# Performance work log

Hardware: AMD Instinct MI355X
Metric: run time of the kernel (lower is better)

The kernel has to match this reference:

```python
import jax, jax.numpy as jnp
import numpy as np

LEN_C = 1024
LR = 0.01
GAMMA = 0.999
R, S, E = 4, 4, 4


def setup_inputs() -> dict:
    key = jax.random.key(0)
    k1, k2, k3 = jax.random.split(key, 3)
    Fx = jax.random.normal(k1, (R, S, E, LEN_C), dtype=jnp.float32)
    Dis = jax.random.normal(k2, (E, LEN_C), dtype=jnp.float32)
    initial_weights = jax.random.normal(k3, (R, S, LEN_C), dtype=jnp.float32) * 0.02
    return {"Fx": Fx, "Dis": Dis, "initial_weights": initial_weights}


def reference(Fx, Dis, initial_weights):
    len_c = Fx.shape[-1]
    # --- first_grad: one-step adaptation gradient (detached in original torch code) ---
    w0 = jax.lax.stop_gradient(initial_weights)
    anti = jnp.einsum('rsen,rsn->e', Fx, w0)           # [E]
    error = Dis[:, -1] - anti                           # [E]
    # d/dw of sum_e error_e^2 with error = Dis - Fx.w  =>  -2 * Fx^T error
    weights_grad = jax.lax.stop_gradient(-2.0 * jnp.einsum('rsen,e->rsn', Fx, error))
    control_weights = initial_weights - 0.5 * LR * weights_grad  # [R,S,N]
    # --- build_delay_line, vectorized Toeplitz gather:
    # Fx_extend[t, r, s, e, n] = Fx[r, s, e, t-n] if t >= n else 0
    t = jnp.arange(len_c)
    idx = t[:, None] - t[None, :]                       # [T, N]
    mask = idx >= 0
    safe_idx = jnp.where(mask, idx, 0)
    Fx_ext = jnp.where(mask, Fx[..., safe_idx], jnp.float32(0.0))  # [R,S,E,T,N]
    # --- adaptive_filtering: sum over r, s, n ---
    anti_noise_matrix = jnp.einsum('rsetn,rsn->te', Fx_ext, control_weights)  # [T,E]
    gamma_vector = jnp.power(jnp.float32(GAMMA), (len_c - 1 - t).astype(jnp.float32))
    return anti_noise_matrix, gamma_vector
```

## Files before the change

kernel.cpp:

```cpp
#include <hip/hip_runtime.h>

#define LEN_C 1024
#define LR_F 0.01f
#define GAMMA_F 0.999f

__global__ __launch_bounds__(256) void k_fused(const float* __restrict__ Fx,
                                               const float* __restrict__ Dis,
                                               const float* __restrict__ w0,
                                               float* __restrict__ out) {
    int bid = blockIdx.x;
    int tid = threadIdx.x;
    int e = bid / 40;
    int r = bid % 40;
    int Tb, Nb;
    if (r < 4)       { Tb = 0; Nb = r; }
    else if (r < 12) { Tb = 1; Nb = r - 4; }
    else if (r < 24) { Tb = 2; Nb = r - 12; }
    else             { Tb = 3; Nb = r - 24; }
    const int T0 = Tb * 256, N0 = Nb * 64;
    const int B = T0 - N0 - 63;

    __shared__ __align__(16) float sFx[16 * 320];
    __shared__ __align__(16) float sCw[16 * 64];
    __shared__ float sPart[4][4];
    __shared__ float sErr[4];

    if (bid < 4) {
        int g = (bid << 8) + tid;
        out[4 * LEN_C + g] = powf(GAMMA_F, (float)(LEN_C - 1 - g));
    }

    for (int rs = 0; rs < 16; ++rs) {
        const float* src = Fx + (rs * 4 + e) * LEN_C;
        for (int m = tid; m < 320; m += 256) {
            int k = B + m;
            sFx[rs * 320 + m] = ((unsigned)k < (unsigned)LEN_C) ? src[k] : 0.f;
        }
    }

    float a0 = 0.f, a1 = 0.f, a2 = 0.f, a3 = 0.f;
    #pragma unroll 4
    for (int i = tid; i < 4096; i += 256) {
        int rs = i >> 8;
        int n4 = i & 255;
        const float4* fx = (const float4*)(Fx + rs * (4 * LEN_C)) + n4;
        float4 wv = ((const float4*)(w0 + rs * LEN_C))[n4];
        float4 f0 = fx[0], f1 = fx[256], f2 = fx[512], f3 = fx[768];
        a0 += f0.x * wv.x + f0.y * wv.y + f0.z * wv.z + f0.w * wv.w;
        a1 += f1.x * wv.x + f1.y * wv.y + f1.z * wv.z + f1.w * wv.w;
        a2 += f2.x * wv.x + f2.y * wv.y + f2.z * wv.z + f2.w * wv.w;
        a3 += f3.x * wv.x + f3.y * wv.y + f3.z * wv.z + f3.w * wv.w;
    }
    for (int off = 32; off > 0; off >>= 1) {
        a0 += __shfl_down(a0, off, 64);
        a1 += __shfl_down(a1, off, 64);
        a2 += __shfl_down(a2, off, 64);
        a3 += __shfl_down(a3, off, 64);
    }
    int w = tid >> 6, l = tid & 63;
    if (l == 0) { sPart[w][0] = a0; sPart[w][1] = a1; sPart[w][2] = a2; sPart[w][3] = a3; }
    __syncthreads();
    if (tid < 4) {
        float anti = sPart[0][tid] + sPart[1][tid] + sPart[2][tid] + sPart[3][tid];
        sErr[tid] = Dis[tid * LEN_C + (LEN_C - 1)] - anti;
    }
    __syncthreads();

    {
        int rs = tid >> 4, j4 = (tid & 15) * 4;
        int n = N0 + j4;
        const float* base = Fx + rs * (4 * LEN_C) + n;
        float4 wv = *(const float4*)(w0 + rs * LEN_C + n);
        float4 f0 = *(const float4*)(base);
        float4 f1 = *(const float4*)(base + LEN_C);
        float4 f2 = *(const float4*)(base + 2 * LEN_C);
        float4 f3 = *(const float4*)(base + 3 * LEN_C);
        float e0 = sErr[0], e1 = sErr[1], e2 = sErr[2], e3 = sErr[3];
        float4 c;
        c.x = wv.x + LR_F * (f0.x * e0 + f1.x * e1 + f2.x * e2 + f3.x * e3);
        c.y = wv.y + LR_F * (f0.y * e0 + f1.y * e1 + f2.y * e2 + f3.y * e3);
        c.z = wv.z + LR_F * (f0.z * e0 + f1.z * e1 + f2.z * e2 + f3.z * e3);
        c.w = wv.w + LR_F * (f0.w * e0 + f1.w * e1 + f2.w * e2 + f3.w * e3);
        *(float4*)(sCw + rs * 64 + j4) = c;
    }
    __syncthreads();

    int i0 = l * 4;
    float acc0 = 0.f, acc1 = 0.f, acc2 = 0.f, acc3 = 0.f;
    #pragma unroll
    for (int rr = 0; rr < 4; ++rr) {
        int rs = (w << 2) + rr;
        const float* crow = sCw + rs * 64;
        const float* frow = sFx + rs * 320;
        int M = i0 + 60;
        float4 flo = *(const float4*)(frow + M);
        float4 fhi = *(const float4*)(frow + M + 4);
        #pragma unroll
        for (int jb = 0; jb < 16; ++jb) {
            float4 c = *(const float4*)(crow + (jb << 2));
            float v0 = flo.x, v1 = flo.y, v2 = flo.z, v3 = flo.w;
            float v4 = fhi.x, v5 = fhi.y, v6 = fhi.z;
            acc0 += v3 * c.x + v2 * c.y + v1 * c.z + v0 * c.w;
            acc1 += v4 * c.x + v3 * c.y + v2 * c.z + v1 * c.w;
            acc2 += v5 * c.x + v4 * c.y + v3 * c.z + v2 * c.w;
            acc3 += v6 * c.x + v5 * c.y + v4 * c.z + v3 * c.w;
            fhi = flo;
            M -= 4;
            if (jb < 15) flo = *(const float4*)(frow + M);
        }
    }

    __syncthreads();
    float* sred = sFx;
    sred[w * 256 + i0 + 0] = acc0;
    sred[w * 256 + i0 + 1] = acc1;
    sred[w * 256 + i0 + 2] = acc2;
    sred[w * 256 + i0 + 3] = acc3;
    __syncthreads();
    float sum = sred[tid] + sred[256 + tid] + sred[512 + tid] + sred[768 + tid];
    atomicAdd(&out[(T0 + tid) * 4 + e], sum);
}

extern "C" void kernel_launch(void* const* d_in, const int* in_sizes, int n_in,
                              void* d_out, int out_size, void* d_ws, size_t ws_size,
                              hipStream_t stream) {
    const float* Fx  = (const float*)d_in[0];
    const float* Dis = (const float*)d_in[1];
    const float* w0  = (const float*)d_in[2];
    float* out = (float*)d_out;

    k_fused<<<160, 256, 0, stream>>>(Fx, Dis, w0, out);
}
```

Baseline: 72.26 us.

## Split fused kernel into single-block prep and 640-block convolution kernel

Moves the error and control-weight computation into a separate one-block kernel that writes the control weights to workspace. The convolution kernel no longer recomputes the global dot-product reduction in every block. It also splits the rs dimension into four groups, so it launches 640 smaller blocks with less shared memory each. The cost is a second kernel launch, a serial dependency on a single-block kernel, and four times as many atomicAdds into the output.

```diff
diff --git a/kernel.cpp b/kernel.cpp
--- a/kernel.cpp
+++ b/kernel.cpp
@@ -4,14 +4,79 @@
 #define LR_F 0.01f
 #define GAMMA_F 0.999f
 
-__global__ __launch_bounds__(256) void k_fused(const float* __restrict__ Fx,
+__global__ __launch_bounds__(1024) void k_prep(const float* __restrict__ Fx,
                                                const float* __restrict__ Dis,
                                                const float* __restrict__ w0,
+                                               float* __restrict__ cw,
                                                float* __restrict__ out) {
-    int bid = blockIdx.x;
-    int tid = threadIdx.x;
-    int e = bid / 40;
-    int r = bid % 40;
+    const int tid = threadIdx.x;
+    const int w = tid >> 6;
+    const int l = tid & 63;
+
+    __shared__ float sP[16][4];
+    __shared__ float sErr[4];
+
+    out[4 * LEN_C + tid] = powf(GAMMA_F, (float)(LEN_C - 1 - tid));
+
+    const float4* wp = (const float4*)(w0 + w * LEN_C);
+    const float4* fp = (const float4*)(Fx + w * 4 * LEN_C);
+    float4 wv[4], fv[4][4];
+    #pragma unroll
+    for (int k = 0; k < 4; ++k) wv[k] = wp[l + 64 * k];
+    #pragma unroll
+    for (int e = 0; e < 4; ++e)
+        #pragma unroll
+        for (int k = 0; k < 4; ++k) fv[e][k] = fp[e * 256 + l + 64 * k];
+
+    float a[4];
+    #pragma unroll
+    for (int e = 0; e < 4; ++e) {
+        float s = 0.f;
+        #pragma unroll
+        for (int k = 0; k < 4; ++k)
+            s += fv[e][k].x * wv[k].x + fv[e][k].y * wv[k].y +
+                 fv[e][k].z * wv[k].z + fv[e][k].w * wv[k].w;
+        a[e] = s;
+    }
+    #pragma unroll
+    for (int off = 32; off > 0; off >>= 1) {
+        a[0] += __shfl_down(a[0], off, 64);
+        a[1] += __shfl_down(a[1], off, 64);
+        a[2] += __shfl_down(a[2], off, 64);
+        a[3] += __shfl_down(a[3], off, 64);
+    }
+    if (l == 0) { sP[w][0] = a[0]; sP[w][1] = a[1]; sP[w][2] = a[2]; sP[w][3] = a[3]; }
+    __syncthreads();
+    if (tid < 4) {
+        float anti = 0.f;
+        #pragma unroll
+        for (int rs = 0; rs < 16; ++rs) anti += sP[rs][tid];
+        sErr[tid] = Dis[tid * LEN_C + (LEN_C - 1)] - anti;
+    }
+    __syncthreads();
+
+    const float e0 = sErr[0], e1 = sErr[1], e2 = sErr[2], e3 = sErr[3];
+    float4* cwp = (float4*)(cw + w * LEN_C);
+    #pragma unroll
+    for (int k = 0; k < 4; ++k) {
+        float4 c;
+        c.x = wv[k].x + LR_F * (fv[0][k].x * e0 + fv[1][k].x * e1 + fv[2][k].x * e2 + fv[3][k].x * e3);
+        c.y = wv[k].y + LR_F * (fv[0][k].y * e0 + fv[1][k].y * e1 + fv[2][k].y * e2 + fv[3][k].y * e3);
+        c.z = wv[k].z + LR_F * (fv[0][k].z * e0 + fv[1][k].z * e1 + fv[2][k].z * e2 + fv[3][k].z * e3);
+        c.w = wv[k].w + LR_F * (fv[0][k].w * e0 + fv[1][k].w * e1 + fv[2][k].w * e2 + fv[3][k].w * e3);
+        cwp[l + 64 * k] = c;
+    }
+}
+
+__global__ __launch_bounds__(256) void k_conv(const float* __restrict__ Fx,
+                                              const float* __restrict__ cw,
+                                              float* __restrict__ out) {
+    const int bid = blockIdx.x;
+    const int tid = threadIdx.x;
+    const int g = bid & 3;
+    const int r = (bid >> 2) % 40;
+    const int e = bid / 160;
+
     int Tb, Nb;
     if (r < 4)       { Tb = 0; Nb = r; }
     else if (r < 12) { Tb = 1; Nb = r - 4; }
@@ -20,78 +85,26 @@
     const int T0 = Tb * 256, N0 = Nb * 64;
     const int B = T0 - N0 - 63;
 
-    __shared__ __align__(16) float sFx[16 * 320];
-    __shared__ __align__(16) float sCw[16 * 64];
-    __shared__ float sPart[4][4];
-    __shared__ float sErr[4];
+    __shared__ __align__(16) float sFx[4 * 320];
+    __shared__ __align__(16) float sCw[4 * 64];
 
-    if (bid < 4) {
-        int g = (bid << 8) + tid;
-        out[4 * LEN_C + g] = powf(GAMMA_F, (float)(LEN_C - 1 - g));
-    }
-
-    for (int rs = 0; rs < 16; ++rs) {
-        const float* src = Fx + (rs * 4 + e) * LEN_C;
+    #pragma unroll
+    for (int rr = 0; rr < 4; ++rr) {
+        const float* src = Fx + ((g * 4 + rr) * 4 + e) * LEN_C;
         for (int m = tid; m < 320; m += 256) {
             int k = B + m;
-            sFx[rs * 320 + m] = ((unsigned)k < (unsigned)LEN_C) ? src[k] : 0.f;
+            sFx[rr * 320 + m] = ((unsigned)k < (unsigned)LEN_C) ? src[k] : 0.f;
         }
     }
-
-    float a0 = 0.f, a1 = 0.f, a2 = 0.f, a3 = 0.f;
-    #pragma unroll 4
-    for (int i = tid; i < 4096; i += 256) {
-        int rs = i >> 8;
-        int n4 = i & 255;
-        const float4* fx = (const float4*)(Fx + rs * (4 * LEN_C)) + n4;
-        float4 wv = ((const float4*)(w0 + rs * LEN_C))[n4];
-        float4 f0 = fx[0], f1 = fx[256], f2 = fx[512], f3 = fx[768];
-        a0 += f0.x * wv.x + f0.y * wv.y + f0.z * wv.z + f0.w * wv.w;
-        a1 += f1.x * wv.x + f1.y * wv.y + f1.z * wv.z + f1.w * wv.w;
-        a2 += f2.x * wv.x + f2.y * wv.y + f2.z * wv.z + f2.w * wv.w;
-        a3 += f3.x * wv.x + f3.y * wv.y + f3.z * wv.z + f3.w * wv.w;
-    }
-    for (int off = 32; off > 0; off >>= 1) {
-        a0 += __shfl_down(a0, off, 64);
-        a1 += __shfl_down(a1, off, 64);
-        a2 += __shfl_down(a2, off, 64);
-        a3 += __shfl_down(a3, off, 64);
-    }
-    int w = tid >> 6, l = tid & 63;
-    if (l == 0) { sPart[w][0] = a0; sPart[w][1] = a1; sPart[w][2] = a2; sPart[w][3] = a3; }
-    __syncthreads();
-    if (tid < 4) {
-        float anti = sPart[0][tid] + sPart[1][tid] + sPart[2][tid] + sPart[3][tid];
-        sErr[tid] = Dis[tid * LEN_C + (LEN_C - 1)] - anti;
-    }
+    sCw[tid] = cw[(g * 4 + (tid >> 6)) * LEN_C + N0 + (tid & 63)];
     __syncthreads();
 
+    const int w = tid >> 6, l = tid & 63;
+    const int i0 = l * 4;
+    float acc0 = 0.f, acc1 = 0.f, acc2 = 0.f, acc3 = 0.f;
     {
-        int rs = tid >> 4, j4 = (tid & 15) * 4;
-        int n = N0 + j4;
-        const float* base = Fx + rs * (4 * LEN_C) + n;
-        float4 wv = *(const float4*)(w0 + rs * LEN_C + n);
-        float4 f0 = *(const float4*)(base);
-        float4 f1 = *(const float4*)(base + LEN_C);
-        float4 f2 = *(const float4*)(base + 2 * LEN_C);
-        float4 f3 = *(const float4*)(base + 3 * LEN_C);
-        float e0 = sErr[0], e1 = sErr[1], e2 = sErr[2], e3 = sErr[3];
-        float4 c;
-        c.x = wv.x + LR_F * (f0.x * e0 + f1.x * e1 + f2.x * e2 + f3.x * e3);
-        c.y = wv.y + LR_F * (f0.y * e0 + f1.y * e1 + f2.y * e2 + f3.y * e3);
-        c.z = wv.z + LR_F * (f0.z * e0 + f1.z * e1 + f2.z * e2 + f3.z * e3);
-        c.w = wv.w + LR_F * (f0.w * e0 + f1.w * e1 + f2.w * e2 + f3.w * e3);
-        *(float4*)(sCw + rs * 64 + j4) = c;
-    }
-    __syncthreads();
-
-    int i0 = l * 4;
-    float acc0 = 0.f, acc1 = 0.f, acc2 = 0.f, acc3 = 0.f;
-    #pragma unroll
-    for (int rr = 0; rr < 4; ++rr) {
-        int rs = (w << 2) + rr;
-        const float* crow = sCw + rs * 64;
-        const float* frow = sFx + rs * 320;
+        const float* crow = sCw + w * 64;
+        const float* frow = sFx + w * 320;
         int M = i0 + 60;
         float4 flo = *(const float4*)(frow + M);
         float4 fhi = *(const float4*)(frow + M + 4);
@@ -128,6 +141,8 @@
     const float* Dis = (const float*)d_in[1];
     const float* w0  = (const float*)d_in[2];
     float* out = (float*)d_out;
+    float* cw  = (float*)d_ws;
 
-    k_fused<<<160, 256, 0, stream>>>(Fx, Dis, w0, out);
+    k_prep<<<1, 1024, 0, stream>>>(Fx, Dis, w0, cw, out);
+    k_conv<<<640, 256, 0, stream>>>(Fx, cw, out);
 }
```

After: 71.48 us. About the same (-1.1%).
